# Kernel tuning notes

Hardware: AMD Instinct MI355X
Metric: run time of the kernel (lower is better)

The kernel has to match this reference:

```python
import jax, jax.numpy as jnp
import numpy as np

PH, PW, SP, C, FH, FW = 7, 7, 4, 10, 34, 34
STRIDE = 8.0


def setup_inputs() -> dict:
    key = jax.random.key(0)
    k1, k2, k3, k4, k5 = jax.random.split(key, 5)
    ft = jax.random.normal(k1, (1, C * PH * PW, FH, FW), dtype=jnp.float32)
    N = 10000
    # rois: (batch_idx, x1, y1, x2, y2) in image coords (im ~ 270x270)
    x1 = jax.random.uniform(k2, (N,), dtype=jnp.float32) * 240.0
    y1 = jax.random.uniform(k3, (N,), dtype=jnp.float32) * 240.0
    w = 8.0 + jax.random.uniform(k4, (N,), dtype=jnp.float32) * 80.0
    h = 8.0 + jax.random.uniform(k5, (N,), dtype=jnp.float32) * 80.0
    rois = jnp.stack([jnp.zeros((N,), jnp.float32), x1, y1,
                      jnp.minimum(x1 + w, 269.0), jnp.minimum(y1 + h, 269.0)], axis=1)
    return {"ft_add_left_right": ft, "rois": rois}


def reference(ft_add_left_right, rois):
    N = rois.shape[0]
    # [PH, PW, FH, FW, C] position-sensitive feature map
    feat = jnp.transpose(ft_add_left_right[0].reshape(C, PH, PW, FH, FW), (1, 2, 3, 4, 0))

    rsw = rois[:, 1] / STRIDE
    rsh = rois[:, 2] / STRIDE
    rew = rois[:, 3] / STRIDE
    reh = rois[:, 4] / STRIDE
    roi_h = jnp.where(reh - rsh > 0.1, reh - rsh, 0.1)  # torch.threshold(x, 0.1, 0.1)
    roi_w = jnp.where(rew - rsw > 0.1, rew - rsw, 0.1)
    bin_h, bin_w = roi_h / PH, roi_w / PW
    sub_h, sub_w = bin_h / SP, bin_w / SP

    pidx = jnp.arange(PH, dtype=jnp.float32)
    sidx = jnp.arange(SP, dtype=jnp.float32) + 0.5
    # sample coords: h [N, PH, SP], w [N, PW, SP]
    hstart = jnp.floor(rsh[:, None] + pidx[None, :] * bin_h[:, None])
    wstart = jnp.floor(rsw[:, None] + pidx[None, :] * bin_w[:, None])
    h = hstart[:, :, None] + sidx[None, None, :] * sub_h[:, None, None]
    w = wstart[:, :, None] + sidx[None, None, :] * sub_w[:, None, None]

    # broadcast to [N, PH, PW, SP(h), SP(w)]
    Hc = h[:, :, None, :, None]
    Wc = w[:, None, :, None, :]
    keep = (Wc > -1) & (Wc < FW) & (Hc > -1) & (Hc < FH)  # [N,PH,PW,SP,SP]

    x1f, y1f = jnp.floor(Wc), jnp.floor(Hc)
    x2f, y2f = jnp.ceil(Wc), jnp.ceil(Hc)
    dx, dy = Wc - x1f, Hc - y1f
    x1, x2 = x1f.astype(jnp.int32), x2f.astype(jnp.int32)
    y1, y2 = y1f.astype(jnp.int32), y2f.astype(jnp.int32)
    x1v, x2v = (x1 >= 0) & (x1 < FW), (x2 >= 0) & (x2 < FW)
    y1v, y2v = (y1 >= 0) & (y1 < FH), (y2 >= 0) & (y2 < FH)
    x1c, x2c = jnp.clip(x1, 0, FW - 1), jnp.clip(x2, 0, FW - 1)
    y1c, y2c = jnp.clip(y1, 0, FH - 1), jnp.clip(y2, 0, FH - 1)

    phidx = jnp.arange(PH)[None, :, None, None, None]
    pwidx = jnp.arange(PW)[None, None, :, None, None]

    def corner(yi, xi, valid, wgt):
        v = feat[phidx, pwidx, yi, xi]  # [N,PH,PW,SP,SP,C]
        m = (wgt * valid.astype(wgt.dtype))
        return v * m[..., None]

    value = (corner(y1c, x1c, x1v & y1v, (1 - dx) * (1 - dy))
             + corner(y2c, x1c, x1v & y2v, (1 - dx) * dy)
             + corner(y1c, x2c, x2v & y1v, dx * (1 - dy))
             + corner(y2c, x2c, x2v & y2v, dx * dy))
    keep_f = keep.astype(value.dtype)
    sum_ = jnp.sum(value * keep_f[..., None], axis=(3, 4))  # [N,PH,PW,C]
    count = jnp.sum(keep_f, axis=(3, 4))                    # [N,PH,PW]
    result = jnp.where(count[..., None] > 0, sum_ / jnp.maximum(count, 1.0)[..., None], 0.0)
    # bins ordered ph*PW + pw -> [N, C, 49]
    return jnp.transpose(result.reshape(N, PH * PW, C), (0, 2, 1))
```

## Files before the change

kernel.cpp:

```cpp
#include <hip/hip_runtime.h>

#define PH 7
#define PW 7
#define SP 4
#define C 10
#define FH 34
#define FW 34
#define NBIN (PH*PW)
#define PLANE (FH*FW)
#define NP (NBIN*PLANE)
#define RPB 512
#define NOUTC (C*NBIN)
#define TJ 16
#define PADW 17

struct AxisW { float w0, w1, w2; int base; };

__device__ __forceinline__ AxisW axis_weights(float rs, float re, int p, int F) {
#pragma clang fp contract(off)
    float d  = re - rs;
    float sp = (d > 0.1f) ? d : 0.1f;
    float bs = sp / 7.0f;
    float ss = bs / 4.0f;
    float st = floorf(rs + (float)p * bs);
    int   B0 = (int)floorf(st);

    float w0 = 0.f, w1 = 0.f, w2 = 0.f; int cnt = 0;
#pragma unroll
    for (int s = 0; s < SP; ++s) {
        float v = st + ((float)s + 0.5f) * ss;
        if (v > -1.0f && v < (float)F) {
            ++cnt;
            float f1 = floorf(v);
            float dv = v - f1;
            int   i1 = (int)f1;
            int   i2 = (int)ceilf(v);
            float a  = (1.0f - dv) * ((i1 >= 0 && i1 < F) ? 1.0f : 0.0f);
            float b  = dv          * ((i2 >= 0 && i2 < F) ? 1.0f : 0.0f);
            int o1 = i1 - B0;
            int o2 = i2 - B0;
            w0 += (o1 == 0) ? a : 0.0f;
            w1 += (o1 == 1) ? a : 0.0f;
            w1 += (o2 == 1) ? b : 0.0f;
            w2 += (o2 == 2) ? b : 0.0f;
        }
    }
    float rc = (cnt > 0) ? 1.0f / (float)cnt : 0.0f;
    w0 *= rc; w1 *= rc; w2 *= rc;

    int Bc = min(max(B0, 0), F - 3);
    int dB = B0 - Bc;
    int m0 = 0 - dB, m1 = 1 - dB, m2 = 2 - dB;
    AxisW out;
    out.w0 = (m0 == 0) ? w0 : (m0 == 1) ? w1 : (m0 == 2) ? w2 : 0.0f;
    out.w1 = (m1 == 0) ? w0 : (m1 == 1) ? w1 : (m1 == 2) ? w2 : 0.0f;
    out.w2 = (m2 == 0) ? w0 : (m2 == 1) ? w1 : (m2 == 2) ? w2 : 0.0f;
    out.base = Bc;
    return out;
}

__global__ __launch_bounds__(RPB, 6) void roi_kernel(const float* __restrict__ ft,
                                                     const float* __restrict__ rois,
                                                     float* __restrict__ ws2,
                                                     int N, int blocksPerBin) {
    __shared__ float4 ldsA[PLANE * 2];
    __shared__ float2 ldsB[PLANE];

    const int bin   = blockIdx.x / blocksPerBin;
    const int chunk = blockIdx.x % blocksPerBin;
    const int tid   = threadIdx.x;
    const int ph    = bin / PW;
    const int pw    = bin % PW;

    {
        const float* base = ft + (size_t)bin * PLANE;
        for (int idx = tid; idx < 2 * PLANE; idx += RPB) {
            int yx = idx >> 1;
            int q  = idx & 1;
            const float* b0 = base + (size_t)(q * 4) * NP + yx;
            float4 v;
            v.x = b0[0];
            v.y = b0[NP];
            v.z = b0[2 * NP];
            v.w = b0[3 * NP];
            ldsA[idx] = v;
        }
        const float* b8 = base + (size_t)8 * NP;
        for (int yx = tid; yx < PLANE; yx += RPB) {
            float2 v;
            v.x = b8[yx];
            v.y = b8[NP + yx];
            ldsB[yx] = v;
        }
    }

    const int n = chunk * RPB + tid;
    const int nv = (n < N) ? n : 0;
    const float* r = rois + nv * 5;
    float rx1 = r[1] * 0.125f;
    float ry1 = r[2] * 0.125f;
    float rx2 = r[3] * 0.125f;
    float ry2 = r[4] * 0.125f;
    AxisW H = axis_weights(ry1, ry2, ph, FH);
    AxisW W = axis_weights(rx1, rx2, pw, FW);
    const int base = H.base * FW + W.base;
    float rw[3] = {H.w0, H.w1, H.w2};
    float cw[3] = {W.w0, W.w1, W.w2};

    __syncthreads();

    if (n >= N) return;

    float4 a0 = make_float4(0.f,0.f,0.f,0.f);
    float4 a1 = make_float4(0.f,0.f,0.f,0.f);
    float  a8 = 0.f, a9 = 0.f;
#pragma unroll
    for (int j = 0; j < 3; ++j) {
        float wy = rw[j];
#pragma unroll
        for (int i = 0; i < 3; ++i) {
            float w = wy * cw[i];
            int pix = base + j * FW + i;
            float4 f0 = ldsA[pix * 2];
            float4 f1 = ldsA[pix * 2 + 1];
            float2 f2 = ldsB[pix];
            a0.x += w * f0.x; a0.y += w * f0.y; a0.z += w * f0.z; a0.w += w * f0.w;
            a1.x += w * f1.x; a1.y += w * f1.y; a1.z += w * f1.z; a1.w += w * f1.w;
            a8   += w * f2.x; a9   += w * f2.y;
        }
    }

    float* o = ws2 + (size_t)(bin * C) * N + n;
    o[0 * (size_t)N] = a0.x;
    o[1 * (size_t)N] = a0.y;
    o[2 * (size_t)N] = a0.z;
    o[3 * (size_t)N] = a0.w;
    o[4 * (size_t)N] = a1.x;
    o[5 * (size_t)N] = a1.y;
    o[6 * (size_t)N] = a1.z;
    o[7 * (size_t)N] = a1.w;
    o[8 * (size_t)N] = a8;
    o[9 * (size_t)N] = a9;
}

__global__ __launch_bounds__(256) void transpose_out(const float* __restrict__ ws2,
                                                     float* __restrict__ out, int N) {
    __shared__ float t[NOUTC * PADW];
    int n0  = blockIdx.x * TJ;
    int tid = threadIdx.x;
    bool fast = (n0 + TJ <= N) && ((N & 3) == 0);

    if (fast) {
        const float4* ws4 = (const float4*)ws2;
        int N4  = N >> 2;
        int n04 = n0 >> 2;
        for (int idx = tid; idx < NOUTC * (TJ / 4); idx += 256) {
            int r = idx >> 2;
            int k = idx & 3;
            float4 v = ws4[(size_t)r * N4 + n04 + k];
            float* dst = &t[r * PADW + 4 * k];
            dst[0] = v.x; dst[1] = v.y; dst[2] = v.z; dst[3] = v.w;
        }
    } else {
        for (int idx = tid; idx < NOUTC * TJ; idx += 256) {
            int r = idx / TJ;
            int j = idx - r * TJ;
            int n = n0 + j;
            t[r * PADW + j] = (n < N) ? ws2[(size_t)r * N + n] : 0.0f;
        }
    }
    __syncthreads();

    if (fast) {
        float2* out2 = (float2*)out;
        for (int idx = tid; idx < TJ * (NOUTC / 2); idx += 256) {
            int j  = idx / (NOUTC / 2);
            int t2 = idx - j * (NOUTC / 2);
            int col0 = 2 * t2, col1 = col0 + 1;
            int c0 = col0 / NBIN, b0 = col0 - c0 * NBIN;
            int c1 = col1 / NBIN, b1 = col1 - c1 * NBIN;
            float2 v;
            v.x = t[(b0 * C + c0) * PADW + j];
            v.y = t[(b1 * C + c1) * PADW + j];
            out2[(size_t)(n0 + j) * (NOUTC / 2) + t2] = v;
        }
    } else {
        for (int idx = tid; idx < TJ * NOUTC; idx += 256) {
            int j   = idx / NOUTC;
            int col = idx - j * NOUTC;
            int c   = col / NBIN;
            int b   = col - c * NBIN;
            int n   = n0 + j;
            if (n < N) out[(size_t)n * NOUTC + col] = t[(b * C + c) * PADW + j];
        }
    }
}

__global__ __launch_bounds__(256) void roi_direct(const float* __restrict__ ft,
                                                  const float* __restrict__ rois,
                                                  float* __restrict__ out, int N) {
#pragma clang fp contract(off)
    int tid = blockIdx.x * blockDim.x + threadIdx.x;
    if (tid >= N * NBIN) return;
    int bin = tid % NBIN;
    int n   = tid / NBIN;
    int ph  = bin / PW;
    int pw  = bin % PW;
    const float* r = rois + n * 5;
    float rsw = r[1]*0.125f, rsh = r[2]*0.125f, rew = r[3]*0.125f, reh = r[4]*0.125f;
    AxisW H = axis_weights(rsh, reh, ph, FH);
    AxisW W = axis_weights(rsw, rew, pw, FW);
    float rw[3] = {H.w0, H.w1, H.w2};
    float cw[3] = {W.w0, W.w1, W.w2};
    float acc[C];
    for (int c = 0; c < C; ++c) acc[c] = 0.0f;
    const float* base = ft + (size_t)bin * PLANE;
    for (int j = 0; j < 3; ++j) {
        int y = H.base + j;
        for (int i = 0; i < 3; ++i) {
            int x = W.base + i;
            float w = rw[j] * cw[i];
            int off = y * FW + x;
            for (int c = 0; c < C; ++c)
                acc[c] += w * base[(size_t)c * NP + off];
        }
    }
    float* o = out + (size_t)n * NOUTC + bin;
    for (int c = 0; c < C; ++c) o[c * NBIN] = acc[c];
}

extern "C" void kernel_launch(void* const* d_in, const int* in_sizes, int n_in,
                              void* d_out, int out_size, void* d_ws, size_t ws_size,
                              hipStream_t stream) {
    const float* ft   = (const float*)d_in[0];
    const float* rois = (const float*)d_in[1];
    float* out = (float*)d_out;
    int N = in_sizes[1] / 5;

    size_t need = (size_t)NOUTC * N * sizeof(float);

    if (ws_size >= need) {
        float* ws2 = (float*)d_ws;
        int blocksPerBin = (N + RPB - 1) / RPB;
        roi_kernel<<<NBIN * blocksPerBin, RPB, 0, stream>>>(ft, rois, ws2,
                                                            N, blocksPerBin);
        int tblocks = (N + TJ - 1) / TJ;
        transpose_out<<<tblocks, 256, 0, stream>>>(ws2, out, N);
    } else {
        int total = N * NBIN;
        roi_direct<<<(total + 255) / 256, 256, 0, stream>>>(ft, rois, out, N);
    }
}
```

Baseline: 90.58 us.

## Store intermediate workspace as packed bf16 and reorganize transpose staging

Measured after the change: 81.16 us. 1.12x faster.

```diff
diff --git a/kernel.cpp b/kernel.cpp
--- a/kernel.cpp
+++ b/kernel.cpp
@@ -9,10 +9,24 @@
 #define NBIN (PH*PW)
 #define PLANE (FH*FW)
 #define NP (NBIN*PLANE)
-#define RPB 512
+#define RPB 1024
 #define NOUTC (C*NBIN)
+#define NR (NOUTC/2)
 #define TJ 16
-#define PADW 17
+
+__device__ __forceinline__ unsigned int pack_bf2(float lo, float hi) {
+    unsigned int a = __float_as_uint(lo);
+    a += 0x7FFFu + ((a >> 16) & 1u);
+    unsigned int b = __float_as_uint(hi);
+    b += 0x7FFFu + ((b >> 16) & 1u);
+    return (a >> 16) | (b & 0xFFFF0000u);
+}
+__device__ __forceinline__ float bf2f_lo(unsigned int u) {
+    return __uint_as_float(u << 16);
+}
+__device__ __forceinline__ float bf2f_hi(unsigned int u) {
+    return __uint_as_float(u & 0xFFFF0000u);
+}
 
 struct AxisW { float w0, w1, w2; int base; };
 
@@ -59,9 +73,9 @@
     return out;
 }
 
-__global__ __launch_bounds__(RPB, 6) void roi_kernel(const float* __restrict__ ft,
+__global__ __launch_bounds__(RPB, 8) void roi_kernel(const float* __restrict__ ft,
                                                      const float* __restrict__ rois,
-                                                     float* __restrict__ ws2,
+                                                     unsigned int* __restrict__ ws2,
                                                      int N, int blocksPerBin) {
     __shared__ float4 ldsA[PLANE * 2];
     __shared__ float2 ldsB[PLANE];
@@ -130,68 +144,65 @@
         }
     }
 
-    float* o = ws2 + (size_t)(bin * C) * N + n;
-    o[0 * (size_t)N] = a0.x;
-    o[1 * (size_t)N] = a0.y;
-    o[2 * (size_t)N] = a0.z;
-    o[3 * (size_t)N] = a0.w;
-    o[4 * (size_t)N] = a1.x;
-    o[5 * (size_t)N] = a1.y;
-    o[6 * (size_t)N] = a1.z;
-    o[7 * (size_t)N] = a1.w;
-    o[8 * (size_t)N] = a8;
-    o[9 * (size_t)N] = a9;
-}
-
-__global__ __launch_bounds__(256) void transpose_out(const float* __restrict__ ws2,
+    unsigned int* o = ws2 + (size_t)(bin * 5) * N + n;
+    o[0 * (size_t)N] = pack_bf2(a0.x, a0.y);
+    o[1 * (size_t)N] = pack_bf2(a0.z, a0.w);
+    o[2 * (size_t)N] = pack_bf2(a1.x, a1.y);
+    o[3 * (size_t)N] = pack_bf2(a1.z, a1.w);
+    o[4 * (size_t)N] = pack_bf2(a8,   a9);
+}
+
+__global__ __launch_bounds__(256) void transpose_out(const unsigned int* __restrict__ ws2,
                                                      float* __restrict__ out, int N) {
-    __shared__ float t[NOUTC * PADW];
+    __shared__ __align__(16) float t[TJ * NOUTC];
     int n0  = blockIdx.x * TJ;
     int tid = threadIdx.x;
     bool fast = (n0 + TJ <= N) && ((N & 3) == 0);
 
     if (fast) {
-        const float4* ws4 = (const float4*)ws2;
-        int N4  = N >> 2;
-        int n04 = n0 >> 2;
-        for (int idx = tid; idx < NOUTC * (TJ / 4); idx += 256) {
+        for (int idx = tid; idx < NR * 4; idx += 256) {
             int r = idx >> 2;
-            int k = idx & 3;
-            float4 v = ws4[(size_t)r * N4 + n04 + k];
-            float* dst = &t[r * PADW + 4 * k];
-            dst[0] = v.x; dst[1] = v.y; dst[2] = v.z; dst[3] = v.w;
+            int q = idx & 3;
+            uint4 v = *(const uint4*)(ws2 + (size_t)r * N + n0 + q * 4);
+            int bin  = r / 5;
+            int k    = r - bin * 5;
+            int col0 = (2 * k) * NBIN + bin;
+            float* tb = &t[(q * 4) * NOUTC + col0];
+            tb[0 * NOUTC]        = bf2f_lo(v.x);
+            tb[0 * NOUTC + NBIN] = bf2f_hi(v.x);
+            tb[1 * NOUTC]        = bf2f_lo(v.y);
+            tb[1 * NOUTC + NBIN] = bf2f_hi(v.y);
+            tb[2 * NOUTC]        = bf2f_lo(v.z);
+            tb[2 * NOUTC + NBIN] = bf2f_hi(v.z);
+            tb[3 * NOUTC]        = bf2f_lo(v.w);
+            tb[3 * NOUTC + NBIN] = bf2f_hi(v.w);
         }
     } else {
-        for (int idx = tid; idx < NOUTC * TJ; idx += 256) {
+        for (int idx = tid; idx < NR * TJ; idx += 256) {
             int r = idx / TJ;
             int j = idx - r * TJ;
             int n = n0 + j;
-            t[r * PADW + j] = (n < N) ? ws2[(size_t)r * N + n] : 0.0f;
+            unsigned int v = (n < N) ? ws2[(size_t)r * N + n] : 0u;
+            int bin  = r / 5;
+            int k    = r - bin * 5;
+            int col0 = (2 * k) * NBIN + bin;
+            t[j * NOUTC + col0]        = bf2f_lo(v);
+            t[j * NOUTC + col0 + NBIN] = bf2f_hi(v);
         }
     }
     __syncthreads();
 
     if (fast) {
-        float2* out2 = (float2*)out;
-        for (int idx = tid; idx < TJ * (NOUTC / 2); idx += 256) {
-            int j  = idx / (NOUTC / 2);
-            int t2 = idx - j * (NOUTC / 2);
-            int col0 = 2 * t2, col1 = col0 + 1;
-            int c0 = col0 / NBIN, b0 = col0 - c0 * NBIN;
-            int c1 = col1 / NBIN, b1 = col1 - c1 * NBIN;
-            float2 v;
-            v.x = t[(b0 * C + c0) * PADW + j];
-            v.y = t[(b1 * C + c1) * PADW + j];
-            out2[(size_t)(n0 + j) * (NOUTC / 2) + t2] = v;
-        }
+        const float4* t4  = (const float4*)t;
+        float4* out4 = (float4*)(out + (size_t)n0 * NOUTC);
+        for (int idx = tid; idx < TJ * NOUTC / 4; idx += 256)
+            out4[idx] = t4[idx];
     } else {
         for (int idx = tid; idx < TJ * NOUTC; idx += 256) {
             int j   = idx / NOUTC;
             int col = idx - j * NOUTC;
-            int c   = col / NBIN;
-            int b   = col - c * NBIN;
             int n   = n0 + j;
-            if (n < N) out[(size_t)n * NOUTC + col] = t[(b * C + c) * PADW + j];
+            if (n < N) out[(size_t)n * NOUTC + col] = t[j * NOUTC + col];
         }
     }
 }
@@ -237,10 +248,10 @@
     float* out = (float*)d_out;
     int N = in_sizes[1] / 5;
 
-    size_t need = (size_t)NOUTC * N * sizeof(float);
+    size_t need = (size_t)NR * N * sizeof(unsigned int);
 
     if (ws_size >= need) {
-        float* ws2 = (float*)d_ws;
+        unsigned int* ws2 = (unsigned int*)d_ws;
         int blocksPerBin = (N + RPB - 1) / RPB;
         roi_kernel<<<NBIN * blocksPerBin, RPB, 0, stream>>>(ft, rois, ws2,
                                                             N, blocksPerBin);
```
